# Kernel tuning notes

Hardware: AMD Instinct MI355X
Metric: run time of the kernel (lower is better)

Reference implementation:

```python
import jax, jax.numpy as jnp
import numpy as np

NEG_INF = -10000000000.0
TEMPERATURE = 0.5
N_NODES = 100000
N_EDGES = 3200000
DIM = 32


def setup_inputs() -> dict:
    key = jax.random.key(0)
    ks = jax.random.split(key, 8)
    node_reps = jax.random.normal(ks[0], (N_NODES, DIM), dtype=jnp.float32)
    edge_reps = jax.random.normal(ks[1], (N_EDGES, DIM), dtype=jnp.float32)
    graph_rep = jax.random.normal(ks[2], (DIM,), dtype=jnp.float32)
    subgraph_rep = jax.random.normal(ks[3], (DIM,), dtype=jnp.float32)
    W1 = jax.random.normal(ks[4], (3 * DIM, DIM), dtype=jnp.float32) / np.sqrt(3 * DIM)
    b1 = jax.random.normal(ks[5], (DIM,), dtype=jnp.float32) * 0.01
    edge_index = jax.random.randint(ks[6], (2, N_EDGES), 0, N_NODES, dtype=jnp.int64)
    selection = jax.random.randint(ks[7], (N_EDGES,), 0, 2) > 0
    return {"node_reps": node_reps, "edge_reps": edge_reps, "graph_rep": graph_rep,
            "subgraph_rep": subgraph_rep, "W1": W1, "b1": b1,
            "edge_index": edge_index, "selection": selection}


def reference(node_reps, edge_reps, graph_rep, subgraph_rep, W1, b1, edge_index, selection):
    # gather per-edge endpoint reps: [E, 32] each
    src = node_reps[edge_index[0]]
    dst = node_reps[edge_index[1]]
    tmp = jnp.concatenate([src, dst, edge_reps], axis=1)  # [E, 96]
    edge_action_reps = jax.nn.elu(tmp @ W1 + b1)          # Linear(96,32)+ELU
    graph_diff_rep = graph_rep - subgraph_rep             # [32]
    score = edge_action_reps @ graph_diff_rep             # [E]
    score = jnp.where(selection, NEG_INF, score)          # mask already-selected edges
    return jax.nn.softmax(score / TEMPERATURE)
```

## Files before the change

### kernel.cpp

```cpp
#include <hip/hip_runtime.h>

#define E_EDGES 3200000
#define N_NODES_K 100000
#define NEG_INF_F (-10000000000.0f)
#define KE_NB (E_EDGES / 256)

typedef __attribute__((ext_vector_type(8))) short short8v;
typedef __attribute__((ext_vector_type(4))) float floatx4;

__device__ __forceinline__ unsigned packbf2(float a, float b) {
    unsigned ua = __float_as_uint(a), ub = __float_as_uint(b);
    ua = (ua + 0x7fffu + ((ua >> 16) & 1u)) >> 16;
    ub = (ub + 0x7fffu + ((ub >> 16) & 1u)) & 0xffff0000u;
    return ub | ua;
}

__global__ __launch_bounds__(256) void k_nodeproj(
    const float* __restrict__ nr, const float* __restrict__ W1,
    const float* __restrict__ b1, unsigned* __restrict__ P1c,
    unsigned* __restrict__ P2c, const unsigned* __restrict__ ei_w,
    const unsigned* __restrict__ sel_w, int* __restrict__ flags) {
    if (blockIdx.x == 0 && threadIdx.x < 64) {
        const int lane = threadIdx.x;
        unsigned hw = ei_w[2 * (lane + 1) + 1];
        unsigned long long anyhi = __ballot(hw != 0u);
        unsigned sv = sel_w[lane];
        unsigned long long not01 = __ballot(sv != 0u && sv != 1u);
        unsigned long long notf  = __ballot(sv != 0u && sv != 0x3F800000u);
        if (lane == 0) {
            flags[0] = (anyhi == 0ull) ? 1 : 0;
            flags[1] = (not01 == 0ull) ? 0 : ((notf == 0ull) ? 2 : 1);
        }
    }
    int n = blockIdx.x * 256 + threadIdx.x;
    if (n >= N_NODES_K) return;
    const float4* x4 = (const float4*)(nr + (size_t)n * 32);
    float xr[32];
#pragma unroll
    for (int i = 0; i < 8; ++i) {
        float4 t = x4[i];
        xr[4 * i + 0] = t.x; xr[4 * i + 1] = t.y; xr[4 * i + 2] = t.z; xr[4 * i + 3] = t.w;
    }
    float a1[32], a2[32];
#pragma unroll
    for (int j = 0; j < 32; ++j) { a1[j] = b1[j]; a2[j] = 0.0f; }
#pragma unroll
    for (int k = 0; k < 32; ++k) {
        const float xv = xr[k];
#pragma unroll
        for (int jb = 0; jb < 8; ++jb) {
            const float4 w1 = *(const float4*)(W1 + (size_t)k * 32 + jb * 4);
            const float4 w2 = *(const float4*)(W1 + (size_t)(32 + k) * 32 + jb * 4);
            a1[4 * jb + 0] = fmaf(xv, w1.x, a1[4 * jb + 0]);
            a1[4 * jb + 1] = fmaf(xv, w1.y, a1[4 * jb + 1]);
            a1[4 * jb + 2] = fmaf(xv, w1.z, a1[4 * jb + 2]);
            a1[4 * jb + 3] = fmaf(xv, w1.w, a1[4 * jb + 3]);
            a2[4 * jb + 0] = fmaf(xv, w2.x, a2[4 * jb + 0]);
            a2[4 * jb + 1] = fmaf(xv, w2.y, a2[4 * jb + 1]);
            a2[4 * jb + 2] = fmaf(xv, w2.z, a2[4 * jb + 2]);
            a2[4 * jb + 3] = fmaf(xv, w2.w, a2[4 * jb + 3]);
        }
    }
    unsigned r1[16], r2[16];
#pragma unroll
    for (int j = 0; j < 16; ++j) {
        r1[j] = packbf2(a1[j], a1[j + 16]);
        r2[j] = packbf2(a2[j], a2[j + 16]);
    }
    uint4* o1 = (uint4*)(P1c + (size_t)n * 16);
    uint4* o2 = (uint4*)(P2c + (size_t)n * 16);
#pragma unroll
    for (int i = 0; i < 4; ++i) {
        o1[i] = ((const uint4*)r1)[i];
        o2[i] = ((const uint4*)r2)[i];
    }
}

__global__ __launch_bounds__(256) void k_edge(
    const float* __restrict__ er_, const float* __restrict__ W1,
    const float* __restrict__ gr, const float* __restrict__ sgr,
    const void* __restrict__ ei_raw, const void* __restrict__ sel_raw,
    const int* __restrict__ flags,
    const unsigned* __restrict__ P1c, const unsigned* __restrict__ P2c,
    float* __restrict__ scores, float* __restrict__ bmax,
    float* __restrict__ bsum) {
    __shared__ int sIdx[256];
    __shared__ int dIdx[256];
    __shared__ int aAct[256];
    __shared__ float sred[8];

    const int tid = threadIdx.x;
    const int e0 = blockIdx.x * 256;
    const int fei = flags[0], fsel = flags[1];

    bool act;
    if (fsel == 0)
        act = __builtin_nontemporal_load((const int*)sel_raw + e0 + tid) == 0;
    else if (fsel == 1)
        act = __builtin_nontemporal_load((const unsigned char*)sel_raw + e0 + tid) == 0;
    else
        act = __builtin_nontemporal_load((const float*)sel_raw + e0 + tid) == 0.0f;

    int s = 0, d = 0;
    if (act) {
        if (fei) {
            s = __builtin_nontemporal_load((const int*)ei_raw + 2 * (size_t)(e0 + tid));
            d = __builtin_nontemporal_load((const int*)ei_raw +
                                           2 * ((size_t)E_EDGES + e0 + tid));
        } else {
            s = __builtin_nontemporal_load((const int*)ei_raw + e0 + tid);
            d = __builtin_nontemporal_load((const int*)ei_raw + E_EDGES + e0 + tid);
        }
    }
    sIdx[tid] = s; dIdx[tid] = d; aAct[tid] = act ? 1 : 0;

    const int lane = tid & 63;
    const int wv   = tid >> 6;
    const int col  = lane & 15;
    const int g    = lane >> 4;
    const int kb   = g * 8;

    union { unsigned u[4]; short8v v; } A0, A1;
#pragma unroll
    for (int t = 0; t < 4; ++t) {
        float x0 = W1[(size_t)(64 + kb + 2 * t) * 32 + col];
        float x1 = W1[(size_t)(64 + kb + 2 * t + 1) * 32 + col];
        A0.u[t] = packbf2(x0, x1);
        float y0 = W1[(size_t)(64 + kb + 2 * t) * 32 + 16 + col];
        float y1 = W1[(size_t)(64 + kb + 2 * t + 1) * 32 + 16 + col];
        A1.u[t] = packbf2(y0, y1);
    }
    float gd0[4], gd1[4];
#pragma unroll
    for (int r = 0; r < 4; ++r) {
        gd0[r] = gr[g * 4 + r] - sgr[g * 4 + r];
        gd1[r] = gr[16 + g * 4 + r] - sgr[16 + g * 4 + r];
    }
    __syncthreads();

    float s_loc[4];
#pragma unroll
    for (int t = 0; t < 4; ++t) {
        const int erow = (wv * 4 + t) * 16 + col;
        const bool ea = aAct[erow] != 0;

        union { unsigned u[4]; short8v v; } B;
        B.u[0] = 0u; B.u[1] = 0u; B.u[2] = 0u; B.u[3] = 0u;
        if (ea) {
            const floatx4* ep = (const floatx4*)(er_ + (size_t)(e0 + erow) * 32 + kb);
            floatx4 xa = __builtin_nontemporal_load(ep);
            floatx4 xb = __builtin_nontemporal_load(ep + 1);
            B.u[0] = packbf2(xa.x, xa.y); B.u[1] = packbf2(xa.z, xa.w);
            B.u[2] = packbf2(xb.x, xb.y); B.u[3] = packbf2(xb.z, xb.w);
        }

        floatx4 acc0 = {0.f, 0.f, 0.f, 0.f}, acc1 = {0.f, 0.f, 0.f, 0.f};
        acc0 = __builtin_amdgcn_mfma_f32_16x16x32_bf16(A0.v, B.v, acc0, 0, 0, 0);
        acc1 = __builtin_amdgcn_mfma_f32_16x16x32_bf16(A1.v, B.v, acc1, 0, 0, 0);

        uint4 u1 = make_uint4(0u, 0u, 0u, 0u), u2 = make_uint4(0u, 0u, 0u, 0u);
        if (ea) {
            u1 = *(const uint4*)(P1c + (size_t)sIdx[erow] * 16 + g * 4);
            u2 = *(const uint4*)(P2c + (size_t)dIdx[erow] * 16 + g * 4);
        }
        const unsigned* pu1 = (const unsigned*)&u1;
        const unsigned* pu2 = (const unsigned*)&u2;
        float part = 0.0f;
#pragma unroll
        for (int r = 0; r < 4; ++r) {
            float z0 = acc0[r] + __uint_as_float(pu1[r] << 16)
                               + __uint_as_float(pu2[r] << 16);
            float z1 = acc1[r] + __uint_as_float(pu1[r] & 0xffff0000u)
                               + __uint_as_float(pu2[r] & 0xffff0000u);
            float h0 = z0 > 0.0f ? z0 : (__expf(z0) - 1.0f);
            float h1 = z1 > 0.0f ? z1 : (__expf(z1) - 1.0f);
            part = fmaf(h0, gd0[r], part);
            part = fmaf(h1, gd1[r], part);
        }
        part += __shfl_xor(part, 16);
        part += __shfl_xor(part, 32);
        float sc = ea ? part : NEG_INF_F;
        s_loc[t] = sc;
        if (g == 0) scores[e0 + erow] = sc;
    }

    float m = fmaxf(fmaxf(s_loc[0], s_loc[1]), fmaxf(s_loc[2], s_loc[3]));
#pragma unroll
    for (int off = 32; off > 0; off >>= 1) m = fmaxf(m, __shfl_down(m, off));
    if (lane == 0) sred[wv] = m;
    __syncthreads();
    const float mb = fmaxf(fmaxf(sred[0], sred[1]), fmaxf(sred[2], sred[3]));
    float v = 0.0f;
    if (g == 0) {
#pragma unroll
        for (int t = 0; t < 4; ++t) v += __expf((s_loc[t] - mb) * 2.0f);
    }
#pragma unroll
    for (int off = 32; off > 0; off >>= 1) v += __shfl_down(v, off);
    __syncthreads();
    if (lane == 0) sred[4 + wv] = v;
    __syncthreads();
    if (tid == 0) {
        bmax[blockIdx.x] = mb;
        bsum[blockIdx.x] = sred[4] + sred[5] + sred[6] + sred[7];
    }
}

__global__ __launch_bounds__(256) void k_reduce(
    const float* __restrict__ bmax, const float* __restrict__ bsum,
    float* __restrict__ mx_out, float* __restrict__ rsum_out) {
    const int tid = threadIdx.x;
    __shared__ float sm[4];
    float m = -3.0e38f;
    for (int i = tid; i < KE_NB; i += 256) m = fmaxf(m, bmax[i]);
#pragma unroll
    for (int off = 32; off > 0; off >>= 1) m = fmaxf(m, __shfl_down(m, off));
    const int lane = tid & 63, wid = tid >> 6;
    if (lane == 0) sm[wid] = m;
    __syncthreads();
    const float M = fmaxf(fmaxf(sm[0], sm[1]), fmaxf(sm[2], sm[3]));
    float s = 0.0f;
    for (int i = tid; i < KE_NB; i += 256)
        s += bsum[i] * __expf((bmax[i] - M) * 2.0f);
#pragma unroll
    for (int off = 32; off > 0; off >>= 1) s += __shfl_down(s, off);
    __syncthreads();
    __shared__ float ss[4];
    if (lane == 0) ss[wid] = s;
    __syncthreads();
    if (tid == 0) {
        *mx_out = M;
        *rsum_out = 1.0f / (ss[0] + ss[1] + ss[2] + ss[3]);
    }
}

__global__ __launch_bounds__(256) void k_fin(
    const float* __restrict__ scores, const float* __restrict__ mx,
    const float* __restrict__ rsum, float* __restrict__ out) {
    const int i = blockIdx.x * 256 + threadIdx.x;
    const float M = *mx;
    const float r = *rsum;
    float4 s = ((const float4*)scores)[i];
    float4 o;
    o.x = __expf((s.x - M) * 2.0f) * r;
    o.y = __expf((s.y - M) * 2.0f) * r;
    o.z = __expf((s.z - M) * 2.0f) * r;
    o.w = __expf((s.w - M) * 2.0f) * r;
    ((float4*)out)[i] = o;
}

extern "C" void kernel_launch(void* const* d_in, const int* in_sizes, int n_in,
                              void* d_out, int out_size, void* d_ws, size_t ws_size,
                              hipStream_t stream) {
    const float* node_reps    = (const float*)d_in[0];
    const float* edge_reps    = (const float*)d_in[1];
    const float* graph_rep    = (const float*)d_in[2];
    const float* subgraph_rep = (const float*)d_in[3];
    const float* W1           = (const float*)d_in[4];
    const float* b1           = (const float*)d_in[5];
    const void*  ei           = d_in[6];
    const void*  selp         = d_in[7];
    float* out = (float*)d_out;

    char* ws = (char*)d_ws;
    size_t off = 0;
    unsigned* P1c = (unsigned*)(ws + off); off += (size_t)N_NODES_K * 64;
    unsigned* P2c = (unsigned*)(ws + off); off += (size_t)N_NODES_K * 64;
    float* scores = (float*)(ws + off);    off += (size_t)E_EDGES * 4;
    float* bmax   = (float*)(ws + off);    off += (size_t)KE_NB * 4;
    float* bsum   = (float*)(ws + off);    off += (size_t)KE_NB * 4;
    int*   flags  = (int*)(ws + off);      off += 64;
    float* mx     = (float*)(ws + off);    off += 4;
    float* rsum   = (float*)(ws + off);    off += 4;

    k_nodeproj<<<(N_NODES_K + 255) / 256, 256, 0, stream>>>(
        node_reps, W1, b1, P1c, P2c,
        (const unsigned*)ei, (const unsigned*)selp, flags);
    k_edge<<<KE_NB, 256, 0, stream>>>(edge_reps, W1, graph_rep, subgraph_rep,
                                      ei, selp, flags, P1c, P2c, scores, bmax, bsum);
    k_reduce<<<1, 256, 0, stream>>>(bmax, bsum, mx, rsum);
    k_fin<<<E_EDGES / 4 / 256, 256, 0, stream>>>(scores, mx, rsum, out);
}
```

Measured before the change: 139.3 us.

## Replace LDS staging and block barriers in edge kernel with wave shuffles

The edge kernel no longer stages src/dst indices and active flags in shared memory. It broadcasts them with intra-wave shuffles, which removes every __syncthreads, and it now emits one softmax partial per wave rather than per block. Index loads and edge-rep and projection loads become unconditional, with inactive edges redirected to safe addresses. This drops divergence but adds memory traffic for masked edges (about half of them). The reduce kernel grows to 1024 threads to handle four times as many partials, and the edge kernel gets a launch-bounds occupancy hint.

```diff
diff --git a/kernel.cpp b/kernel.cpp
--- a/kernel.cpp
+++ b/kernel.cpp
@@ -4,6 +4,7 @@
 #define N_NODES_K 100000
 #define NEG_INF_F (-10000000000.0f)
 #define KE_NB (E_EDGES / 256)
+#define NPART (KE_NB * 4)
 
 typedef __attribute__((ext_vector_type(8))) short short8v;
 typedef __attribute__((ext_vector_type(4))) float floatx4;
@@ -76,7 +77,7 @@
     }
 }
 
-__global__ __launch_bounds__(256) void k_edge(
+__global__ __launch_bounds__(256, 4) void k_edge(
     const float* __restrict__ er_, const float* __restrict__ W1,
     const float* __restrict__ gr, const float* __restrict__ sgr,
     const void* __restrict__ ei_raw, const void* __restrict__ sel_raw,
@@ -84,11 +85,6 @@
     const unsigned* __restrict__ P1c, const unsigned* __restrict__ P2c,
     float* __restrict__ scores, float* __restrict__ bmax,
     float* __restrict__ bsum) {
-    __shared__ int sIdx[256];
-    __shared__ int dIdx[256];
-    __shared__ int aAct[256];
-    __shared__ float sred[8];
-
     const int tid = threadIdx.x;
     const int e0 = blockIdx.x * 256;
     const int fei = flags[0], fsel = flags[1];
@@ -101,18 +97,18 @@
     else
         act = __builtin_nontemporal_load((const float*)sel_raw + e0 + tid) == 0.0f;
 
-    int s = 0, d = 0;
-    if (act) {
-        if (fei) {
-            s = __builtin_nontemporal_load((const int*)ei_raw + 2 * (size_t)(e0 + tid));
-            d = __builtin_nontemporal_load((const int*)ei_raw +
-                                           2 * ((size_t)E_EDGES + e0 + tid));
-        } else {
-            s = __builtin_nontemporal_load((const int*)ei_raw + e0 + tid);
-            d = __builtin_nontemporal_load((const int*)ei_raw + E_EDGES + e0 + tid);
-        }
-    }
-    sIdx[tid] = s; dIdx[tid] = d; aAct[tid] = act ? 1 : 0;
+    int s, d;
+    if (fei) {
+        s = __builtin_nontemporal_load((const int*)ei_raw + 2 * (size_t)(e0 + tid));
+        d = __builtin_nontemporal_load((const int*)ei_raw +
+                                       2 * ((size_t)E_EDGES + e0 + tid));
+    } else {
+        s = __builtin_nontemporal_load((const int*)ei_raw + e0 + tid);
+        d = __builtin_nontemporal_load((const int*)ei_raw + E_EDGES + e0 + tid);
+    }
+    s = act ? s : 0;
+    d = act ? d : 0;
+    int ia = act ? 1 : 0;
 
     const int lane = tid & 63;
     const int wv   = tid >> 6;
@@ -136,33 +132,30 @@
         gd0[r] = gr[g * 4 + r] - sgr[g * 4 + r];
         gd1[r] = gr[16 + g * 4 + r] - sgr[16 + g * 4 + r];
     }
-    __syncthreads();
 
     float s_loc[4];
 #pragma unroll
     for (int t = 0; t < 4; ++t) {
-        const int erow = (wv * 4 + t) * 16 + col;
-        const bool ea = aAct[erow] != 0;
-
+        const int src  = t * 16 + col;
+        const int se   = __shfl(s, src);
+        const int de   = __shfl(d, src);
+        const int ea   = __shfl(ia, src);
+        const int erow = wv * 64 + t * 16 + col;
+
+        const size_t rrow = ea ? (size_t)(e0 + erow) : (size_t)e0;
+        const floatx4* ep = (const floatx4*)(er_ + rrow * 32 + kb);
+        floatx4 xa = __builtin_nontemporal_load(ep);
+        floatx4 xb = __builtin_nontemporal_load(ep + 1);
         union { unsigned u[4]; short8v v; } B;
-        B.u[0] = 0u; B.u[1] = 0u; B.u[2] = 0u; B.u[3] = 0u;
-        if (ea) {
-            const floatx4* ep = (const floatx4*)(er_ + (size_t)(e0 + erow) * 32 + kb);
-            floatx4 xa = __builtin_nontemporal_load(ep);
-            floatx4 xb = __builtin_nontemporal_load(ep + 1);
-            B.u[0] = packbf2(xa.x, xa.y); B.u[1] = packbf2(xa.z, xa.w);
-            B.u[2] = packbf2(xb.x, xb.y); B.u[3] = packbf2(xb.z, xb.w);
-        }
+        B.u[0] = packbf2(xa.x, xa.y); B.u[1] = packbf2(xa.z, xa.w);
+        B.u[2] = packbf2(xb.x, xb.y); B.u[3] = packbf2(xb.z, xb.w);
 
         floatx4 acc0 = {0.f, 0.f, 0.f, 0.f}, acc1 = {0.f, 0.f, 0.f, 0.f};
         acc0 = __builtin_amdgcn_mfma_f32_16x16x32_bf16(A0.v, B.v, acc0, 0, 0, 0);
         acc1 = __builtin_amdgcn_mfma_f32_16x16x32_bf16(A1.v, B.v, acc1, 0, 0, 0);
 
-        uint4 u1 = make_uint4(0u, 0u, 0u, 0u), u2 = make_uint4(0u, 0u, 0u, 0u);
-        if (ea) {
-            u1 = *(const uint4*)(P1c + (size_t)sIdx[erow] * 16 + g * 4);
-            u2 = *(const uint4*)(P2c + (size_t)dIdx[erow] * 16 + g * 4);
-        }
+        uint4 u1 = *(const uint4*)(P1c + (size_t)se * 16 + g * 4);
+        uint4 u2 = *(const uint4*)(P2c + (size_t)de * 16 + g * 4);
         const unsigned* pu1 = (const unsigned*)&u1;
         const unsigned* pu2 = (const unsigned*)&u2;
         float part = 0.0f;
@@ -187,9 +180,7 @@
     float m = fmaxf(fmaxf(s_loc[0], s_loc[1]), fmaxf(s_loc[2], s_loc[3]));
 #pragma unroll
     for (int off = 32; off > 0; off >>= 1) m = fmaxf(m, __shfl_down(m, off));
-    if (lane == 0) sred[wv] = m;
-    __syncthreads();
-    const float mb = fmaxf(fmaxf(sred[0], sred[1]), fmaxf(sred[2], sred[3]));
+    const float mb = __shfl(m, 0);
     float v = 0.0f;
     if (g == 0) {
 #pragma unroll
@@ -197,40 +188,41 @@
     }
 #pragma unroll
     for (int off = 32; off > 0; off >>= 1) v += __shfl_down(v, off);
-    __syncthreads();
-    if (lane == 0) sred[4 + wv] = v;
-    __syncthreads();
-    if (tid == 0) {
-        bmax[blockIdx.x] = mb;
-        bsum[blockIdx.x] = sred[4] + sred[5] + sred[6] + sred[7];
-    }
-}
-
-__global__ __launch_bounds__(256) void k_reduce(
+    if (lane == 0) {
+        bmax[blockIdx.x * 4 + wv] = mb;
+        bsum[blockIdx.x * 4 + wv] = v;
+    }
+}
+
+__global__ __launch_bounds__(1024) void k_reduce(
     const float* __restrict__ bmax, const float* __restrict__ bsum,
     float* __restrict__ mx_out, float* __restrict__ rsum_out) {
     const int tid = threadIdx.x;
-    __shared__ float sm[4];
     float m = -3.0e38f;
-    for (int i = tid; i < KE_NB; i += 256) m = fmaxf(m, bmax[i]);
+    for (int i = tid; i < NPART; i += 1024) m = fmaxf(m, bmax[i]);
 #pragma unroll
     for (int off = 32; off > 0; off >>= 1) m = fmaxf(m, __shfl_down(m, off));
+    __shared__ float sm[16];
+    __shared__ float ss[16];
     const int lane = tid & 63, wid = tid >> 6;
     if (lane == 0) sm[wid] = m;
     __syncthreads();
-    const float M = fmaxf(fmaxf(sm[0], sm[1]), fmaxf(sm[2], sm[3]));
-    float s = 0.0f;
-    for (int i = tid; i < KE_NB; i += 256)
-        s += bsum[i] * __expf((bmax[i] - M) * 2.0f);
-#pragma unroll
-    for (int off = 32; off > 0; off >>= 1) s += __shfl_down(s, off);
-    __syncthreads();
-    __shared__ float ss[4];
-    if (lane == 0) ss[wid] = s;
+    float M = -3.0e38f;
+#pragma unroll
+    for (int i = 0; i < 16; ++i) M = fmaxf(M, sm[i]);
+    float sum = 0.0f;
+    for (int i = tid; i < NPART; i += 1024)
+        sum += bsum[i] * __expf((bmax[i] - M) * 2.0f);
+#pragma unroll
+    for (int off = 32; off > 0; off >>= 1) sum += __shfl_down(sum, off);
+    if (lane == 0) ss[wid] = sum;
     __syncthreads();
     if (tid == 0) {
+        float tot = 0.0f;
+#pragma unroll
+        for (int i = 0; i < 16; ++i) tot += ss[i];
         *mx_out = M;
-        *rsum_out = 1.0f / (ss[0] + ss[1] + ss[2] + ss[3]);
+        *rsum_out = 1.0f / tot;
     }
 }
 
@@ -267,8 +259,8 @@
     unsigned* P1c = (unsigned*)(ws + off); off += (size_t)N_NODES_K * 64;
     unsigned* P2c = (unsigned*)(ws + off); off += (size_t)N_NODES_K * 64;
     float* scores = (float*)(ws + off);    off += (size_t)E_EDGES * 4;
-    float* bmax   = (float*)(ws + off);    off += (size_t)KE_NB * 4;
-    float* bsum   = (float*)(ws + off);    off += (size_t)KE_NB * 4;
+    float* bmax   = (float*)(ws + off);    off += (size_t)NPART * 4;
+    float* bsum   = (float*)(ws + off);    off += (size_t)NPART * 4;
     int*   flags  = (int*)(ws + off);      off += 64;
     float* mx     = (float*)(ws + off);    off += 4;
     float* rsum   = (float*)(ws + off);    off += 4;
@@ -278,6 +270,6 @@
         (const unsigned*)ei, (const unsigned*)selp, flags);
     k_edge<<<KE_NB, 256, 0, stream>>>(edge_reps, W1, graph_rep, subgraph_rep,
                                       ei, selp, flags, P1c, P2c, scores, bmax, bsum);
-    k_reduce<<<1, 256, 0, stream>>>(bmax, bsum, mx, rsum);
+    k_reduce<<<1, 1024, 0, stream>>>(bmax, bsum, mx, rsum);
     k_fin<<<E_EDGES / 4 / 256, 256, 0, stream>>>(scores, mx, rsum, out);
 }
```

Result: slower. 149.3 us (+7.2%).
